# Performance work log

Measured on AMD Instinct MI355X. Metric: run time of the kernel, lower is better.

## Reference

```python
import jax, jax.numpy as jnp
import numpy as np

S = 9                      # spiral length
V = [8192, 4096, 2048, 1024, 512]  # verts per level, finest -> latent


def grid_sample_bilinear(feat, grid):
    # feat [B,C,H,W], grid [B,P,2] in [-1,1]; bilinear, align_corners=True
    B, C, H, W = feat.shape
    x = (grid[..., 0] + 1.0) * 0.5 * (W - 1)
    y = (grid[..., 1] + 1.0) * 0.5 * (H - 1)
    x0 = jnp.floor(x); y0 = jnp.floor(y)
    wx = x - x0; wy = y - y0
    x0i = jnp.clip(x0.astype(jnp.int32), 0, W - 1)
    x1i = jnp.clip(x0.astype(jnp.int32) + 1, 0, W - 1)
    y0i = jnp.clip(y0.astype(jnp.int32), 0, H - 1)
    y1i = jnp.clip(y0.astype(jnp.int32) + 1, 0, H - 1)
    featf = feat.reshape(B, C, H * W).transpose(0, 2, 1)  # [B,HW,C]
    def gat(yi, xi):
        return jnp.take_along_axis(featf, (yi * W + xi)[..., None], axis=1)  # [B,P,C]
    w00 = ((1 - wy) * (1 - wx))[..., None]
    w01 = ((1 - wy) * wx)[..., None]
    w10 = (wy * (1 - wx))[..., None]
    w11 = (wy * wx)[..., None]
    return gat(y0i, x0i) * w00 + gat(y0i, x1i) * w01 + gat(y1i, x0i) * w10 + gat(y1i, x1i) * w11


def pool(x, row, col, val):
    # sparse mesh upsample: gather cols, scale, scatter-add into rows
    n_out = row.shape[0] // 3
    g = x[:, col, :] * val[None, :, None]                       # [B,nnz,C]
    return jnp.zeros((x.shape[0], n_out, x.shape[-1]), x.dtype).at[:, row, :].add(g)


def dsconv(x, idx, wd, wp, b):
    # depthwise-separable spiral conv: gather spiral ring, depthwise over S, pointwise mix
    g = x[:, idx]                                # [B,N,S,C]
    dw = jnp.einsum('bnsc,sc->bnc', g, wd)       # depthwise over spiral dim
    return jnp.einsum('bnc,co->bno', dw, wp) + b # pointwise


def _forward(uv, feat, upsample, s0, s1, s2, s3,
             row0, col0, val0, row1, col1, val1, row2, col2, val2, row3, col3, val3,
             wd0, wp0, b0, wd1, wp1, b1, wd2, wp2, b2, wd3, wp3, b3, wdh, wph, bh):
    uvc = jnp.clip((uv - 0.5) * 2.0, -1.0, 1.0)
    x = grid_sample_bilinear(feat, uvc)           # [B,P,C]  (torch: [B,C,P] then permute)
    x = jnp.einsum('vp,bpc->bvc', upsample, x)    # [B,V4,C] latent mesh features
    x = jax.nn.relu(dsconv(pool(x, row3, col3, val3), s3, wd0, wp0, b0))  # [B,1024,512]
    x = jax.nn.relu(dsconv(pool(x, row2, col2, val2), s2, wd1, wp1, b1))  # [B,2048,256]
    x = jax.nn.relu(dsconv(pool(x, row1, col1, val1), s1, wd2, wp2, b2))  # [B,4096,128]
    x = jax.nn.relu(dsconv(pool(x, row0, col0, val0), s0, wd3, wp3, b3))  # [B,8192,64]
    return dsconv(x, s0, wdh, wph, bh)            # [B,8192,3]


def setup_inputs():
    ks = jax.random.split(jax.random.key(0), 64)
    B, P, C, H, W = 8, 21, 512, 32, 32
    inp = {}
    inp['uv'] = jax.random.uniform(ks[0], (B, P, 2), jnp.float32)
    inp['feat'] = jax.random.normal(ks[1], (B, C, H, W), jnp.float32)
    inp['upsample'] = 0.01 * jnp.ones((V[4], P), jnp.float32)
    for i in range(4):
        inp[f's{i}'] = jax.random.randint(ks[2 + i], (V[i], S), 0, V[i])
    for i in range(4):
        nnz = 3 * V[i]
        inp[f'row{i}'] = jax.random.randint(ks[6 + 3 * i], (nnz,), 0, V[i])
        inp[f'col{i}'] = jax.random.randint(ks[7 + 3 * i], (nnz,), 0, V[i + 1])
        inp[f'val{i}'] = jax.random.uniform(ks[8 + 3 * i], (nnz,), jnp.float32)
    chans = [(512, 512), (512, 256), (256, 128), (128, 64), (64, 3)]
    names = ['0', '1', '2', '3', 'h']
    k = 20
    for (ci, co), nm in zip(chans, names):
        inp[f'wd{nm}'] = 0.1 * jax.random.normal(ks[k], (S, ci), jnp.float32); k += 1
        inp[f'wp{nm}'] = jax.random.normal(ks[k], (ci, co), jnp.float32) * (1.0 / float(np.sqrt(ci))); k += 1
        inp[f'b{nm}'] = jnp.zeros((co,), jnp.float32); k += 1
    return inp


def reference(uv, feat, upsample, s0, s1, s2, s3,
              row0, col0, val0, row1, col1, val1, row2, col2, val2, row3, col3, val3,
              wd0, wp0, b0, wd1, wp1, b1, wd2, wp2, b2, wd3, wp3, b3, wdh, wph, bh):
    return _forward(uv, feat, upsample, s0, s1, s2, s3,
                    row0, col0, val0, row1, col1, val1, row2, col2, val2, row3, col3, val3,
                    wd0, wp0, b0, wd1, wp1, b1, wd2, wp2, b2, wd3, wp3, b3, wdh, wph, bh)
```

## Files before the change

kernel.cpp:

```cpp
#include <hip/hip_runtime.h>

#define B_  8
#define P_  21
#define H_  32
#define W_  32

typedef float f32x4 __attribute__((ext_vector_type(4)));
typedef _Float16 f16x8 __attribute__((ext_vector_type(8)));

struct CsrParams {
  const int*   row[4];
  const int*   col[4];
  const float* val[4];
  int*   cnt[4];
  int*   rowptr[4];
  int*   colsout[4];
  float* valsout[4];
  int    nnz[4];
  int    V[4];
};

__global__ void zero_cnt_kernel(int* p, int n) {
  int i = blockIdx.x * 256 + threadIdx.x;
  if (i < n) p[i] = 0;
}

__global__ void count_kernel(CsrParams p) {
  int l = blockIdx.y;
  int k = blockIdx.x * 256 + threadIdx.x;
  if (k < p.nnz[l]) atomicAdd(&p.cnt[l][p.row[l][k]], 1);
}

__global__ void scan_kernel(CsrParams p) {
  int l = blockIdx.x;
  int V = p.V[l];
  int* cnt = p.cnt[l];
  int* rp  = p.rowptr[l];
  int t = threadIdx.x;
  int chunk = V / 256;
  int base = t * chunk;
  int s = 0;
  for (int i = 0; i < chunk; ++i) s += cnt[base + i];
  __shared__ int sm[256];
  sm[t] = s;
  __syncthreads();
  for (int off = 1; off < 256; off <<= 1) {
    int v = (t >= off) ? sm[t - off] : 0;
    __syncthreads();
    sm[t] += v;
    __syncthreads();
  }
  int run = sm[t] - s;
  for (int i = 0; i < chunk; ++i) {
    int c = cnt[base + i];
    rp[base + i]  = run;
    cnt[base + i] = run;
    run += c;
  }
  if (t == 255) rp[V] = run;
}

__global__ void fill_kernel(CsrParams p) {
  int l = blockIdx.y;
  int k = blockIdx.x * 256 + threadIdx.x;
  if (k < p.nnz[l]) {
    int r = p.row[l][k];
    int pos = atomicAdd(&p.cnt[l][r], 1);
    p.colsout[l][pos] = p.col[l][k];
    p.valsout[l][pos] = p.val[l][k];
  }
}

__global__ void sample_kernel(const float* __restrict__ uv,
                              const float* __restrict__ feat,
                              float* __restrict__ xs) {
  int bp = blockIdx.x;
  int b  = bp / P_;
  float u0 = uv[bp * 2 + 0], u1 = uv[bp * 2 + 1];
  float gx = fminf(fmaxf((u0 - 0.5f) * 2.0f, -1.0f), 1.0f);
  float gy = fminf(fmaxf((u1 - 0.5f) * 2.0f, -1.0f), 1.0f);
  float fx = (gx + 1.0f) * 0.5f * (W_ - 1);
  float fy = (gy + 1.0f) * 0.5f * (H_ - 1);
  float x0f = floorf(fx), y0f = floorf(fy);
  float wx = fx - x0f, wy = fy - y0f;
  int x0 = (int)x0f, y0 = (int)y0f;
  int x0i = min(max(x0, 0), W_ - 1), x1i = min(max(x0 + 1, 0), W_ - 1);
  int y0i = min(max(y0, 0), H_ - 1), y1i = min(max(y0 + 1, 0), H_ - 1);
  float w00 = (1.f - wy) * (1.f - wx), w01 = (1.f - wy) * wx;
  float w10 = wy * (1.f - wx),        w11 = wy * wx;
  for (int c = threadIdx.x; c < 512; c += blockDim.x) {
    const float* fb = feat + ((size_t)(b * 512 + c)) * (H_ * W_);
    float v = fb[y0i * W_ + x0i] * w00 + fb[y0i * W_ + x1i] * w01 +
              fb[y1i * W_ + x0i] * w10 + fb[y1i * W_ + x1i] * w11;
    xs[(size_t)bp * 512 + c] = v;
  }
}

__global__ void upsample_kernel(const float* __restrict__ up,
                                const float* __restrict__ xs,
                                float* __restrict__ xu) {
  int v = blockIdx.x, b = blockIdx.y;
  int c4 = threadIdx.x << 2;
  float4 acc = make_float4(0.f, 0.f, 0.f, 0.f);
  for (int p = 0; p < P_; ++p) {
    float u = up[v * P_ + p];
    const float4 xv = *(const float4*)&xs[((size_t)(b * P_ + p)) * 512 + c4];
    acc.x = fmaf(u, xv.x, acc.x);
    acc.y = fmaf(u, xv.y, acc.y);
    acc.z = fmaf(u, xv.z, acc.z);
    acc.w = fmaf(u, xv.w, acc.w);
  }
  *(float4*)&xu[((size_t)(b * 512 + v)) * 512 + c4] = acc;
}

__global__ __launch_bounds__(256) void pool_kernel(
    const float* __restrict__ x,
    const int* __restrict__ rowptr,
    const int* __restrict__ cols,
    const float* __restrict__ vals,
    float* __restrict__ out,
    int Vout, int Vin, int Cin) {
  const int lpr    = Cin >> 3;
  const int lshift = 31 - __clz(lpr);
  const int rpb    = 256 >> lshift;
  const int lr = threadIdx.x >> lshift;
  const int lc = threadIdx.x & (lpr - 1);
  const int b  = blockIdx.x & 7;
  const int n  = (blockIdx.x >> 3) * rpb + lr;
  const int c8 = lc << 3;
  const float* xb = x + (size_t)b * Vin * Cin + c8;
  int j0 = rowptr[n], j1 = rowptr[n + 1];
  float4 a0 = make_float4(0.f, 0.f, 0.f, 0.f);
  float4 a1 = make_float4(0.f, 0.f, 0.f, 0.f);
  for (int j = j0; j < j1; ++j) {
    float v = vals[j];
    const float* xr = xb + (size_t)cols[j] * Cin;
    float4 x0 = *(const float4*)xr;
    float4 x1 = *(const float4*)(xr + 4);
    a0.x = fmaf(v, x0.x, a0.x); a0.y = fmaf(v, x0.y, a0.y);
    a0.z = fmaf(v, x0.z, a0.z); a0.w = fmaf(v, x0.w, a0.w);
    a1.x = fmaf(v, x1.x, a1.x); a1.y = fmaf(v, x1.y, a1.y);
    a1.z = fmaf(v, x1.z, a1.z); a1.w = fmaf(v, x1.w, a1.w);
  }
  float* op = &out[((size_t)b * Vout + n) * Cin + c8];
  *(float4*)op = a0;
  *(float4*)(op + 4) = a1;
}

__global__ __launch_bounds__(256) void dw_split_kernel(
    const float* __restrict__ xin,
    const int* __restrict__ sidx,
    const float* __restrict__ wd,
    _Float16* __restrict__ a0o,
    _Float16* __restrict__ a1o,
    int Vout, int Cin) {
  const int lpr    = Cin >> 3;
  const int lshift = 31 - __clz(lpr);
  const int rpb    = 256 >> lshift;
  const int lr = threadIdx.x >> lshift;
  const int lc = threadIdx.x & (lpr - 1);
  const int b  = blockIdx.x & 7;
  const int n  = (blockIdx.x >> 3) * rpb + lr;
  const int c8 = lc << 3;
  const float* xb = xin + (size_t)b * Vout * Cin + c8;

  int idx[9];
  #pragma unroll
  for (int s = 0; s < 9; ++s) idx[s] = sidx[n * 9 + s];

  float4 a0 = make_float4(0.f, 0.f, 0.f, 0.f);
  float4 a1 = make_float4(0.f, 0.f, 0.f, 0.f);
  #pragma unroll
  for (int s = 0; s < 9; ++s) {
    const float* xr = xb + (size_t)idx[s] * Cin;
    float4 x0 = *(const float4*)xr;
    float4 x1 = *(const float4*)(xr + 4);
    const float* wr = wd + s * Cin + c8;
    float4 w0 = *(const float4*)wr;
    float4 w1 = *(const float4*)(wr + 4);
    a0.x = fmaf(w0.x, x0.x, a0.x); a0.y = fmaf(w0.y, x0.y, a0.y);
    a0.z = fmaf(w0.z, x0.z, a0.z); a0.w = fmaf(w0.w, x0.w, a0.w);
    a1.x = fmaf(w1.x, x1.x, a1.x); a1.y = fmaf(w1.y, x1.y, a1.y);
    a1.z = fmaf(w1.z, x1.z, a1.z); a1.w = fmaf(w1.w, x1.w, a1.w);
  }

  size_t m = (size_t)b * Vout + n;
  float v[8] = {a0.x, a0.y, a0.z, a0.w, a1.x, a1.y, a1.z, a1.w};
  f16x8 hi, lo;
  #pragma unroll
  for (int i = 0; i < 8; ++i) {
    _Float16 h0 = (_Float16)v[i];
    float r = (v[i] - (float)h0) * 2048.0f;
    hi[i] = h0;
    lo[i] = (_Float16)r;
  }
  *(f16x8*)&a0o[m * Cin + c8] = hi;
  *(f16x8*)&a1o[m * Cin + c8] = lo;
}

struct BsplitParams {
  const float* wp[4];
  int K[4], N[4], off[4];
  _Float16* b0;
  _Float16* b1;
};

__global__ void bsplit_all_kernel(BsplitParams p) {
  int idx = blockIdx.x * 256 + threadIdx.x;
  #pragma unroll
  for (int t = 0; t < 4; ++t) {
    int sz = p.N[t] * p.K[t];
    if (idx < sz) {
      int n = idx / p.K[t], k = idx - n * p.K[t];
      float v = p.wp[t][(size_t)k * p.N[t] + n];
      _Float16 h0 = (_Float16)v;
      float r = (v - (float)h0) * 2048.0f;
      p.b0[p.off[t] + idx] = h0;
      p.b1[p.off[t] + idx] = (_Float16)r;
      return;
    }
    idx -= sz;
  }
}

__global__ __launch_bounds__(256) void gemm_f16x2(
    const _Float16* __restrict__ A0, const _Float16* __restrict__ A1,
    const _Float16* __restrict__ Bt0, const _Float16* __restrict__ Bt1,
    const float* __restrict__ bias, float* __restrict__ C,
    int M, int N, int K) {
  constexpr int RP = 72;
  __shared__ _Float16 As[2][128][RP];
  __shared__ _Float16 Bs[2][64][RP];
  const int tid = threadIdx.x;
  const int bx = blockIdx.x;
  const int xr_ = (bx & 7) * (gridDim.x >> 3) + (bx >> 3);
  const int m0 = xr_ * 128, n0 = blockIdx.y * 64;
  const int wid = tid >> 6, lane = tid & 63;
  const int wr = wid >> 1, wc = wid & 1;
  const int lo = lane & 15, hi = lane >> 4;

  f32x4 accM[4][2], accC[4][2];
  #pragma unroll
  for (int mi = 0; mi < 4; ++mi)
    #pragma unroll
    for (int nj = 0; nj < 2; ++nj) {
      accM[mi][nj] = (f32x4){0.f, 0.f, 0.f, 0.f};
      accC[mi][nj] = (f32x4){0.f, 0.f, 0.f, 0.f};
    }

  const _Float16* gA[2] = {A0, A1};
  const _Float16* gB[2] = {Bt0, Bt1};

  for (int k0 = 0; k0 < K; k0 += 64) {
    #pragma unroll
    for (int p = 0; p < 2; ++p) {
      #pragma unroll
      for (int i = 0; i < 4; ++i) {
        int c = tid + 256 * i;
        int r = c >> 3, k8 = (c & 7) << 3;
        uint4 v = *(const uint4*)(gA[p] + (size_t)(m0 + r) * K + k0 + k8);
        *(uint4*)&As[p][r][k8] = v;
      }
      #pragma unroll
      for (int i = 0; i < 2; ++i) {
        int c = tid + 256 * i;
        int r = c >> 3, k8 = (c & 7) << 3;
        uint4 v = *(const uint4*)(gB[p] + (size_t)(n0 + r) * K + k0 + k8);
        *(uint4*)&Bs[p][r][k8] = v;
      }
    }
    __syncthreads();
    #pragma unroll
    for (int s = 0; s < 2; ++s) {
      const int kk = s * 32 + hi * 8;
      f16x8 af[4][2], bf[2][2];
      #pragma unroll
      for (int mi = 0; mi < 4; ++mi) {
        af[mi][0] = *(const f16x8*)&As[0][wr * 64 + mi * 16 + lo][kk];
        af[mi][1] = *(const f16x8*)&As[1][wr * 64 + mi * 16 + lo][kk];
      }
      #pragma unroll
      for (int nj = 0; nj < 2; ++nj) {
        bf[nj][0] = *(const f16x8*)&Bs[0][wc * 32 + nj * 16 + lo][kk];
        bf[nj][1] = *(const f16x8*)&Bs[1][wc * 32 + nj * 16 + lo][kk];
      }
      #pragma unroll
      for (int mi = 0; mi < 4; ++mi)
        #pragma unroll
        for (int nj = 0; nj < 2; ++nj) {
          accM[mi][nj] = __builtin_amdgcn_mfma_f32_16x16x32_f16(
              af[mi][0], bf[nj][0], accM[mi][nj], 0, 0, 0);
          accC[mi][nj] = __builtin_amdgcn_mfma_f32_16x16x32_f16(
              af[mi][0], bf[nj][1], accC[mi][nj], 0, 0, 0);
          accC[mi][nj] = __builtin_amdgcn_mfma_f32_16x16x32_f16(
              af[mi][1], bf[nj][0], accC[mi][nj], 0, 0, 0);
        }
    }
    __syncthreads();
  }

  const float INV = 1.0f / 2048.0f;
  #pragma unroll
  for (int mi = 0; mi < 4; ++mi)
    #pragma unroll
    for (int nj = 0; nj < 2; ++nj) {
      int col = n0 + wc * 32 + nj * 16 + lo;
      float bv = bias[col];
      #pragma unroll
      for (int r = 0; r < 4; ++r) {
        int row = m0 + wr * 64 + mi * 16 + hi * 4 + r;
        float v = accM[mi][nj][r] + accC[mi][nj][r] * INV + bv;
        v = fmaxf(v, 0.f);
        C[(size_t)row * N + col] = v;
      }
    }
}

__global__ __launch_bounds__(256) void head_fused_kernel(
    const float* __restrict__ x,
    const int* __restrict__ sidx,
    const float* __restrict__ wdh,
    const float* __restrict__ wph,
    const float* __restrict__ bh,
    float* __restrict__ out) {
  const int bid  = blockIdx.x;
  const int b    = bid & 7;
  const int wid  = threadIdx.x >> 6;
  const int lane = threadIdx.x & 63;
  const int n    = (bid >> 3) * 4 + wid;
  const float* xb = x + (size_t)b * 8192 * 64 + lane;

  int idx[9];
  #pragma unroll
  for (int s = 0; s < 9; ++s) idx[s] = sidx[n * 9 + s];

  float acc = 0.f;
  #pragma unroll
  for (int s = 0; s < 9; ++s)
    acc = fmaf(wdh[s * 64 + lane], xb[(size_t)idx[s] * 64], acc);

  float a0 = acc * wph[lane * 3 + 0];
  float a1 = acc * wph[lane * 3 + 1];
  float a2 = acc * wph[lane * 3 + 2];
  for (int off = 32; off > 0; off >>= 1) {
    a0 += __shfl_down(a0, off);
    a1 += __shfl_down(a1, off);
    a2 += __shfl_down(a2, off);
  }
  if (lane == 0) {
    size_t row = (size_t)b * 8192 + n;
    out[row * 3 + 0] = a0 + bh[0];
    out[row * 3 + 1] = a1 + bh[1];
    out[row * 3 + 2] = a2 + bh[2];
  }
}

extern "C" void kernel_launch(void* const* d_in, const int* in_sizes, int n_in,
                              void* d_out, int out_size, void* d_ws, size_t ws_size,
                              hipStream_t stream) {
  const float* uv   = (const float*)d_in[0];
  const float* feat = (const float*)d_in[1];
  const float* up   = (const float*)d_in[2];
  const int* sArr[4] = {(const int*)d_in[3], (const int*)d_in[4],
                        (const int*)d_in[5], (const int*)d_in[6]};

  const size_t SLAB = 8ull * 2048 * 512;
  float* Wf = (float*)d_ws;
  float* S0 = Wf;
  float* S1 = Wf + SLAB;
  _Float16* A0 = (_Float16*)(S1 + SLAB);
  _Float16* A1 = A0 + SLAB;
  _Float16* Bt0all = (_Float16*)(S0 + 4500000);
  _Float16* Bt1all = Bt0all + 434176;
  float* xs = (float*)(A1 + SLAB);
  int* ib = (int*)(xs + (size_t)B_ * P_ * 512);

  int Vt[4] = {1024, 2048, 4096, 8192};
  int NZ[4] = {3072, 6144, 12288, 24576};
  int* cnt[4]; int* rp[4]; int* co[4]; float* va[4];
  {
    int* pc = ib;
    for (int t = 0; t < 4; ++t) { cnt[t] = pc; pc += Vt[t]; }
    for (int t = 0; t < 4; ++t) { rp[t] = pc; pc += Vt[t] + 1; }
    for (int t = 0; t < 4; ++t) { co[t] = pc; pc += NZ[t]; }
    float* pv = (float*)pc;
    for (int t = 0; t < 4; ++t) { va[t] = pv; pv += NZ[t]; }
  }

  CsrParams cp;
  for (int t = 0; t < 4; ++t) {
    int i = 3 - t;
    cp.row[t] = (const int*)d_in[7 + 3 * i];
    cp.col[t] = (const int*)d_in[8 + 3 * i];
    cp.val[t] = (const float*)d_in[9 + 3 * i];
    cp.cnt[t] = cnt[t]; cp.rowptr[t] = rp[t];
    cp.colsout[t] = co[t]; cp.valsout[t] = va[t];
    cp.nnz[t] = NZ[t]; cp.V[t] = Vt[t];
  }

  zero_cnt_kernel<<<60, 256, 0, stream>>>(ib, 15360);
  count_kernel<<<dim3(96, 4), 256, 0, stream>>>(cp);
  scan_kernel<<<4, 256, 0, stream>>>(cp);
  fill_kernel<<<dim3(96, 4), 256, 0, stream>>>(cp);

  sample_kernel<<<B_ * P_, 256, 0, stream>>>(uv, feat, xs);
  upsample_kernel<<<dim3(512, B_), 128, 0, stream>>>(up, xs, S0);

  struct Stg { int Vin, Vout, Cin, Cout; const int* s; const float *wd, *wp, *bias; };
  Stg st[4] = {
    {512, 1024, 512, 512, sArr[3], (const float*)d_in[19], (const float*)d_in[20], (const float*)d_in[21]},
    {1024, 2048, 512, 256, sArr[2], (const float*)d_in[22], (const float*)d_in[23], (const float*)d_in[24]},
    {2048, 4096, 256, 128, sArr[1], (const float*)d_in[25], (const float*)d_in[26], (const float*)d_in[27]},
    {4096, 8192, 128, 64, sArr[0], (const float*)d_in[28], (const float*)d_in[29], (const float*)d_in[30]},
  };

  BsplitParams bp;
  int boff = 0;
  for (int t = 0; t < 4; ++t) {
    bp.wp[t] = st[t].wp;
    bp.K[t] = st[t].Cin; bp.N[t] = st[t].Cout;
    bp.off[t] = boff;
    boff += st[t].Cin * st[t].Cout;
  }
  bp.b0 = Bt0all; bp.b1 = Bt1all;
  bsplit_all_kernel<<<(boff + 255) / 256, 256, 0, stream>>>(bp);

  for (int t = 0; t < 4; ++t) {
    int rpb = 2048 / st[t].Cin;
    pool_kernel<<<8 * (st[t].Vout / rpb), 256, 0, stream>>>(
        S0, rp[t], co[t], va[t], S1, st[t].Vout, st[t].Vin, st[t].Cin);
    dw_split_kernel<<<8 * (st[t].Vout / rpb), 256, 0, stream>>>(
        S1, st[t].s, st[t].wd, A0, A1, st[t].Vout, st[t].Cin);
    int M = B_ * st[t].Vout;
    gemm_f16x2<<<dim3(M / 128, st[t].Cout / 64), 256, 0, stream>>>(
        A0, A1, Bt0all + bp.off[t], Bt1all + bp.off[t],
        st[t].bias, S0, M, st[t].Cout, st[t].Cin);
  }

  head_fused_kernel<<<8 * (8192 / 4), 256, 0, stream>>>(
      S0, sArr[0], (const float*)d_in[31], (const float*)d_in[32],
      (const float*)d_in[33], (float*)d_out);
}
```

Measured before the change: 279.9 us.

## Fuse mesh pool and spiral depthwise conv via precomputed composite sparse table

```diff
diff --git a/kernel.cpp b/kernel.cpp
--- a/kernel.cpp
+++ b/kernel.cpp
@@ -68,6 +68,86 @@
     int pos = atomicAdd(&p.cnt[l][r], 1);
     p.colsout[l][pos] = p.col[l][k];
     p.valsout[l][pos] = p.val[l][k];
+  }
+}
+
+struct Csr2Params {
+  const int* sidx[4];
+  const int* rp[4];
+  const int* co[4];
+  const float* va[4];
+  int* kcnt[4];
+  int* rp2[4];
+  long long* tab[4];
+  int V[4];
+};
+
+__global__ void kcnt_kernel(Csr2Params p) {
+  int l = blockIdx.y;
+  int n = blockIdx.x * 256 + threadIdx.x;
+  if (n >= p.V[l]) return;
+  const int* si = p.sidx[l] + n * 9;
+  const int* rp = p.rp[l];
+  int s = 0;
+  #pragma unroll
+  for (int t = 0; t < 9; ++t) {
+    int r = si[t];
+    s += rp[r + 1] - rp[r];
+  }
+  p.kcnt[l][n] = s;
+}
+
+__global__ void scan2_kernel(Csr2Params p) {
+  int l = blockIdx.x;
+  int V = p.V[l];
+  int* cnt = p.kcnt[l];
+  int* rp2 = p.rp2[l];
+  int t = threadIdx.x;
+  int chunk = V / 256;
+  int base = t * chunk;
+  int s = 0;
+  for (int i = 0; i < chunk; ++i) s += cnt[base + i];
+  __shared__ int sm[256];
+  sm[t] = s;
+  __syncthreads();
+  for (int off = 1; off < 256; off <<= 1) {
+    int v = (t >= off) ? sm[t - off] : 0;
+    __syncthreads();
+    sm[t] += v;
+    __syncthreads();
+  }
+  int run = sm[t] - s;
+  for (int i = 0; i < chunk; ++i) {
+    int c = cnt[base + i];
+    rp2[base + i] = run;
+    run += c;
+  }
+  if (t == 255) rp2[V] = run;
+}
+
+__global__ void fill2_kernel(Csr2Params p) {
+  int l = blockIdx.y;
+  int id = blockIdx.x * 256 + threadIdx.x;
+  int V = p.V[l];
+  if (id >= 9 * V) return;
+  int n = id / 9;
+  int s = id - n * 9;
+  const int* si = p.sidx[l] + n * 9;
+  const int* rp = p.rp[l];
+  int off = p.rp2[l][n];
+  for (int t = 0; t < s; ++t) {
+    int r = si[t];
+    off += rp[r + 1] - rp[r];
+  }
+  int r = si[s];
+  int j0 = rp[r], j1 = rp[r + 1];
+  const int* co = p.co[l];
+  const float* va = p.va[l];
+  long long* tab = p.tab[l];
+  for (int j = j0; j < j1; ++j) {
+    unsigned int lo = (unsigned int)(co[j] | (s << 16));
+    unsigned int hi = __float_as_uint(va[j]);
+    tab[off++] = (long long)(((unsigned long long)hi << 32) | lo);
   }
 }
 
@@ -113,12 +193,13 @@
   *(float4*)&xu[((size_t)(b * 512 + v)) * 512 + c4] = acc;
 }
 
-__global__ __launch_bounds__(256) void pool_kernel(
+__global__ __launch_bounds__(256) void dw27_kernel(
     const float* __restrict__ x,
-    const int* __restrict__ rowptr,
-    const int* __restrict__ cols,
-    const float* __restrict__ vals,
-    float* __restrict__ out,
+    const long long* __restrict__ tab,
+    const int* __restrict__ rp2,
+    const float* __restrict__ wd,
+    _Float16* __restrict__ a0o,
+    _Float16* __restrict__ a1o,
     int Vout, int Vin, int Cin) {
   const int lpr    = Cin >> 3;
   const int lshift = 31 - __clz(lpr);
@@ -128,60 +209,65 @@
   const int b  = blockIdx.x & 7;
   const int n  = (blockIdx.x >> 3) * rpb + lr;
   const int c8 = lc << 3;
-  const float* xb = x + (size_t)b * Vin * Cin + c8;
-  int j0 = rowptr[n], j1 = rowptr[n + 1];
+  const float* xb  = x + (size_t)b * Vin * Cin + c8;
+  const float* wdc = wd + c8;
+
+  int e0 = rp2[n], e1 = rp2[n + 1];
   float4 a0 = make_float4(0.f, 0.f, 0.f, 0.f);
   float4 a1 = make_float4(0.f, 0.f, 0.f, 0.f);
-  for (int j = j0; j < j1; ++j) {
-    float v = vals[j];
-    const float* xr = xb + (size_t)cols[j] * Cin;
-    float4 x0 = *(const float4*)xr;
-    float4 x1 = *(const float4*)(xr + 4);
-    a0.x = fmaf(v, x0.x, a0.x); a0.y = fmaf(v, x0.y, a0.y);
-    a0.z = fmaf(v, x0.z, a0.z); a0.w = fmaf(v, x0.w, a0.w);
-    a1.x = fmaf(v, x1.x, a1.x); a1.y = fmaf(v, x1.y, a1.y);
-    a1.z = fmaf(v, x1.z, a1.z); a1.w = fmaf(v, x1.w, a1.w);
-  }
-  float* op = &out[((size_t)b * Vout + n) * Cin + c8];
-  *(float4*)op = a0;
-  *(float4*)(op + 4) = a1;
-}
-
-__global__ __launch_bounds__(256) void dw_split_kernel(
-    const float* __restrict__ xin,
-    const int* __restrict__ sidx,
-    const float* __restrict__ wd,
-    _Float16* __restrict__ a0o,
-    _Float16* __restrict__ a1o,
-    int Vout, int Cin) {
-  const int lpr    = Cin >> 3;
-  const int lshift = 31 - __clz(lpr);
-  const int rpb    = 256 >> lshift;
-  const int lr = threadIdx.x >> lshift;
-  const int lc = threadIdx.x & (lpr - 1);
-  const int b  = blockIdx.x & 7;
-  const int n  = (blockIdx.x >> 3) * rpb + lr;
-  const int c8 = lc << 3;
-  const float* xb = xin + (size_t)b * Vout * Cin + c8;
-
-  int idx[9];
-  #pragma unroll
-  for (int s = 0; s < 9; ++s) idx[s] = sidx[n * 9 + s];
-
-  float4 a0 = make_float4(0.f, 0.f, 0.f, 0.f);
-  float4 a1 = make_float4(0.f, 0.f, 0.f, 0.f);
-  #pragma unroll
-  for (int s = 0; s < 9; ++s) {
-    const float* xr = xb + (size_t)idx[s] * Cin;
-    float4 x0 = *(const float4*)xr;
-    float4 x1 = *(const float4*)(xr + 4);
-    const float* wr = wd + s * Cin + c8;
-    float4 w0 = *(const float4*)wr;
-    float4 w1 = *(const float4*)(wr + 4);
-    a0.x = fmaf(w0.x, x0.x, a0.x); a0.y = fmaf(w0.y, x0.y, a0.y);
-    a0.z = fmaf(w0.z, x0.z, a0.z); a0.w = fmaf(w0.w, x0.w, a0.w);
-    a1.x = fmaf(w1.x, x1.x, a1.x); a1.y = fmaf(w1.y, x1.y, a1.y);
-    a1.z = fmaf(w1.z, x1.z, a1.z); a1.w = fmaf(w1.w, x1.w, a1.w);
+
+  int e = e0;
+  for (; e + 3 <= e1; e += 3) {
+    long long v0 = __builtin_nontemporal_load(&tab[e]);
+    long long v1 = __builtin_nontemporal_load(&tab[e + 1]);
+    long long v2 = __builtin_nontemporal_load(&tab[e + 2]);
+    int col0 = (int)((unsigned long long)v0 & 0xFFFF);
+    int col1 = (int)((unsigned long long)v1 & 0xFFFF);
+    int col2 = (int)((unsigned long long)v2 & 0xFFFF);
+    int s0 = (int)(((unsigned long long)v0 >> 16) & 0xFF);
+    int s1 = (int)(((unsigned long long)v1 >> 16) & 0xFF);
+    int s2 = (int)(((unsigned long long)v2 >> 16) & 0xFF);
+    float val0 = __uint_as_float((unsigned int)((unsigned long long)v0 >> 32));
+    float val1 = __uint_as_float((unsigned int)((unsigned long long)v1 >> 32));
+    float val2 = __uint_as_float((unsigned int)((unsigned long long)v2 >> 32));
+    const float* xr0 = xb + (size_t)col0 * Cin;
+    const float* xr1 = xb + (size_t)col1 * Cin;
+    const float* xr2 = xb + (size_t)col2 * Cin;
+    float4 p00 = *(const float4*)xr0, p01 = *(const float4*)(xr0 + 4);
+    float4 p10 = *(const float4*)xr1, p11 = *(const float4*)(xr1 + 4);
+    float4 p20 = *(const float4*)xr2, p21 = *(const float4*)(xr2 + 4);
+    const float* wr0 = wdc + s0 * Cin;
+    const float* wr1 = wdc + s1 * Cin;
+    const float* wr2 = wdc + s2 * Cin;
+    float4 w00 = *(const float4*)wr0, w01 = *(const float4*)(wr0 + 4);
+    float4 w10 = *(const float4*)wr1, w11 = *(const float4*)(wr1 + 4);
+    float4 w20 = *(const float4*)wr2, w21 = *(const float4*)(wr2 + 4);
+    a0.x = fmaf(val0 * w00.x, p00.x, a0.x); a0.y = fmaf(val0 * w00.y, p00.y, a0.y);
+    a0.z = fmaf(val0 * w00.z, p00.z, a0.z); a0.w = fmaf(val0 * w00.w, p00.w, a0.w);
+    a1.x = fmaf(val0 * w01.x, p01.x, a1.x); a1.y = fmaf(val0 * w01.y, p01.y, a1.y);
+    a1.z = fmaf(val0 * w01.z, p01.z, a1.z); a1.w = fmaf(val0 * w01.w, p01.w, a1.w);
+    a0.x = fmaf(val1 * w10.x, p10.x, a0.x); a0.y = fmaf(val1 * w10.y, p10.y, a0.y);
+    a0.z = fmaf(val1 * w10.z, p10.z, a0.z); a0.w = fmaf(val1 * w10.w, p10.w, a0.w);
+    a1.x = fmaf(val1 * w11.x, p11.x, a1.x); a1.y = fmaf(val1 * w11.y, p11.y, a1.y);
+    a1.z = fmaf(val1 * w11.z, p11.z, a1.z); a1.w = fmaf(val1 * w11.w, p11.w, a1.w);
+    a0.x = fmaf(val2 * w20.x, p20.x, a0.x); a0.y = fmaf(val2 * w20.y, p20.y, a0.y);
+    a0.z = fmaf(val2 * w20.z, p20.z, a0.z); a0.w = fmaf(val2 * w20.w, p20.w, a0.w);
+    a1.x = fmaf(val2 * w21.x, p21.x, a1.x); a1.y = fmaf(val2 * w21.y, p21.y, a1.y);
+    a1.z = fmaf(val2 * w21.z, p21.z, a1.z); a1.w = fmaf(val2 * w21.w, p21.w, a1.w);
+  }
+  for (; e < e1; ++e) {
+    long long v0 = __builtin_nontemporal_load(&tab[e]);
+    int col0 = (int)((unsigned long long)v0 & 0xFFFF);
+    int s0 = (int)(((unsigned long long)v0 >> 16) & 0xFF);
+    float val0 = __uint_as_float((unsigned int)((unsigned long long)v0 >> 32));
+    const float* xr0 = xb + (size_t)col0 * Cin;
+    float4 p00 = *(const float4*)xr0, p01 = *(const float4*)(xr0 + 4);
+    const float* wr0 = wdc + s0 * Cin;
+    float4 w00 = *(const float4*)wr0, w01 = *(const float4*)(wr0 + 4);
+    a0.x = fmaf(val0 * w00.x, p00.x, a0.x); a0.y = fmaf(val0 * w00.y, p00.y, a0.y);
+    a0.z = fmaf(val0 * w00.z, p00.z, a0.z); a0.w = fmaf(val0 * w00.w, p00.w, a0.w);
+    a1.x = fmaf(val0 * w01.x, p01.x, a1.x); a1.y = fmaf(val0 * w01.y, p01.y, a1.y);
+    a1.z = fmaf(val0 * w01.z, p01.z, a1.z); a1.w = fmaf(val0 * w01.w, p01.w, a1.w);
   }
 
   size_t m = (size_t)b * Vout + n;
@@ -378,6 +464,7 @@
   int Vt[4] = {1024, 2048, 4096, 8192};
   int NZ[4] = {3072, 6144, 12288, 24576};
   int* cnt[4]; int* rp[4]; int* co[4]; float* va[4];
+  int* kcnt[4]; int* rp2[4];
   {
     int* pc = ib;
     for (int t = 0; t < 4; ++t) { cnt[t] = pc; pc += Vt[t]; }
@@ -385,6 +472,14 @@
     for (int t = 0; t < 4; ++t) { co[t] = pc; pc += NZ[t]; }
     float* pv = (float*)pc;
     for (int t = 0; t < 4; ++t) { va[t] = pv; pv += NZ[t]; }
+    pc = (int*)pv;
+    for (int t = 0; t < 4; ++t) { kcnt[t] = pc; pc += Vt[t]; }
+    for (int t = 0; t < 4; ++t) { rp2[t] = pc; pc += Vt[t] + 1; }
+  }
+  long long* tab[4];
+  {
+    long long* pt = (long long*)S1;
+    for (int t = 0; t < 4; ++t) { tab[t] = pt; pt += 48ull * Vt[t]; }
   }
 
   CsrParams cp;
@@ -398,10 +493,21 @@
     cp.nnz[t] = NZ[t]; cp.V[t] = Vt[t];
   }
 
+  Csr2Params c2;
+  for (int t = 0; t < 4; ++t) {
+    c2.sidx[t] = sArr[3 - t];
+    c2.rp[t] = rp[t]; c2.co[t] = co[t]; c2.va[t] = va[t];
+    c2.kcnt[t] = kcnt[t]; c2.rp2[t] = rp2[t]; c2.tab[t] = tab[t];
+    c2.V[t] = Vt[t];
+  }
+
   zero_cnt_kernel<<<60, 256, 0, stream>>>(ib, 15360);
   count_kernel<<<dim3(96, 4), 256, 0, stream>>>(cp);
   scan_kernel<<<4, 256, 0, stream>>>(cp);
   fill_kernel<<<dim3(96, 4), 256, 0, stream>>>(cp);
+  kcnt_kernel<<<dim3(32, 4), 256, 0, stream>>>(c2);
+  scan2_kernel<<<4, 256, 0, stream>>>(c2);
+  fill2_kernel<<<dim3(288, 4), 256, 0, stream>>>(c2);
 
   sample_kernel<<<B_ * P_, 256, 0, stream>>>(uv, feat, xs);
   upsample_kernel<<<dim3(512, B_), 128, 0, stream>>>(up, xs, S0);
@@ -427,10 +533,9 @@
 
   for (int t = 0; t < 4; ++t) {
     int rpb = 2048 / st[t].Cin;
-    pool_kernel<<<8 * (st[t].Vout / rpb), 256, 0, stream>>>(
-        S0, rp[t], co[t], va[t], S1, st[t].Vout, st[t].Vin, st[t].Cin);
-    dw_split_kernel<<<8 * (st[t].Vout / rpb), 256, 0, stream>>>(
-        S1, st[t].s, st[t].wd, A0, A1, st[t].Vout, st[t].Cin);
+    dw27_kernel<<<8 * (st[t].Vout / rpb), 256, 0, stream>>>(
+        S0, tab[t], rp2[t], st[t].wd, A0, A1,
+        st[t].Vout, st[t].Vin, st[t].Cin);
     int M = B_ * st[t].Vout;
     gemm_f16x2<<<dim3(M / 128, st[t].Cout / 64), 256, 0, stream>>>(
         A0, A1, Bt0all + bp.off[t], Bt1all + bp.off[t],
```

Result: slower. 519.8 us (+85.7%).
